# Optimization experiments

Hardware: AMD Instinct MI355X
Metric: run time of the kernel (lower is better)

Reference implementation:

```python
import jax, jax.numpy as jnp
import numpy as np

D_MODEL = 1024
NHEAD = 16
D_HEAD = D_MODEL // NHEAD


def setup_inputs() -> dict:
    key = jax.random.key(0)
    ks = jax.random.split(key, 11)
    B, S = 4, 1024
    s = 1.0 / np.sqrt(D_MODEL)
    inp = {
        'q_in': jax.random.normal(ks[0], (B, S, D_MODEL), jnp.float32),
        'k_in': jax.random.normal(ks[1], (B, S, D_MODEL), jnp.float32),
        'v_in': jax.random.normal(ks[2], (B, S, D_MODEL), jnp.float32),
        'Wq': jax.random.normal(ks[3], (D_MODEL, D_MODEL), jnp.float32) * s,
        'bq': jnp.zeros((D_MODEL,), jnp.float32),
        'Wk': jax.random.normal(ks[4], (D_MODEL, D_MODEL), jnp.float32) * s,
        'bk': jnp.zeros((D_MODEL,), jnp.float32),
        'Wv': jax.random.normal(ks[5], (D_MODEL, D_MODEL), jnp.float32) * s,
        'bv': jnp.zeros((D_MODEL,), jnp.float32),
        'Wo': jax.random.normal(ks[6], (D_MODEL, D_MODEL), jnp.float32) * s,
        'bo': jnp.zeros((D_MODEL,), jnp.float32),
    }
    return inp


def reference(q_in, k_in, v_in, Wq, bq, Wk, bk, Wv, bv, Wo, bo):
    B, Sq, _ = q_in.shape
    Sk = k_in.shape[1]
    # Linear projections (torch Linear: x @ W.T + b; here W stored as [in, out])
    Q = q_in @ Wq + bq
    K = k_in @ Wk + bk
    V = v_in @ Wv + bv
    # [B, H, S, Dh]
    Qh = Q.reshape(B, Sq, NHEAD, D_HEAD).transpose(0, 2, 1, 3)
    Kh = K.reshape(B, Sk, NHEAD, D_HEAD).transpose(0, 2, 1, 3)
    Vh = V.reshape(B, Sk, NHEAD, D_HEAD).transpose(0, 2, 1, 3)
    scores = jnp.einsum('bhqd,bhkd->bhqk', Qh, Kh) / jnp.sqrt(jnp.float32(D_HEAD))
    attn_weights = jax.nn.softmax(scores, axis=-1)
    attn = jnp.einsum('bhqk,bhkd->bhqd', attn_weights, Vh)
    attn = attn.transpose(0, 2, 1, 3).reshape(B, Sq, D_MODEL)
    out = attn @ Wo + bo
    return out
```

## Files before the change

### kernel.cpp

```cpp
#include <hip/hip_runtime.h>
#include <hip/hip_bf16.h>
#include <cstdint>
#include <cstddef>

typedef __bf16 bf16_t;
typedef __bf16 bf16x8 __attribute__((ext_vector_type(8)));
typedef __bf16 bf16x4 __attribute__((ext_vector_type(4)));
typedef float f32x4 __attribute__((ext_vector_type(4)));

#define DM 1024
#define NHEAD 16
#define DHEAD 64

#define QSCALE 0.18033688011112042f
#define PSHIFT 4.0f
#define RS 72

__device__ __forceinline__ void gload_lds16(const void* g, void* l) {
    __builtin_amdgcn_global_load_lds(
        (const __attribute__((address_space(1))) void*)g,
        (__attribute__((address_space(3))) void*)l,
        16, 0, 0);
}

__global__ void cast3_f32_to_bf16(
    const float* __restrict__ x0, const float* __restrict__ x1, const float* __restrict__ x2,
    bf16_t* __restrict__ y0, bf16_t* __restrict__ y1, bf16_t* __restrict__ y2, int n)
{
    const float* x = blockIdx.z == 0 ? x0 : blockIdx.z == 1 ? x1 : x2;
    bf16_t* y      = blockIdx.z == 0 ? y0 : blockIdx.z == 1 ? y1 : y2;
    int i = (blockIdx.x * blockDim.x + threadIdx.x) * 4;
    if (i < n) {
        float4 v = *(const float4*)&x[i];
        union { bf16_t b[4]; ushort4 u; } o;
        o.b[0] = (bf16_t)v.x; o.b[1] = (bf16_t)v.y; o.b[2] = (bf16_t)v.z; o.b[3] = (bf16_t)v.w;
        *(ushort4*)&y[i] = o.u;
    }
}

__global__ void transpose_cast_w4(
    const float* __restrict__ w0, const float* __restrict__ w1,
    const float* __restrict__ w2, const float* __restrict__ w3,
    bf16_t* __restrict__ t0, bf16_t* __restrict__ t1,
    bf16_t* __restrict__ t2, bf16_t* __restrict__ t3)
{
    const float* w = blockIdx.z == 0 ? w0 : blockIdx.z == 1 ? w1 : blockIdx.z == 2 ? w2 : w3;
    bf16_t* wt     = blockIdx.z == 0 ? t0 : blockIdx.z == 1 ? t1 : blockIdx.z == 2 ? t2 : t3;
    __shared__ float tile[32][33];
    int bx = blockIdx.x * 32;
    int by = blockIdx.y * 32;
    int tx = threadIdx.x, ty = threadIdx.y;
    for (int j = 0; j < 32; j += 8)
        tile[ty + j][tx] = w[(size_t)(by + ty + j) * DM + bx + tx];
    __syncthreads();
    for (int j = 0; j < 32; j += 8)
        wt[(size_t)(bx + ty + j) * DM + by + tx] = (bf16_t)tile[tx][ty + j];
}

template <int MODE>
__device__ __forceinline__ void gemm_body(
    const bf16_t* __restrict__ A, const bf16_t* __restrict__ Bt,
    const float* __restrict__ bias, float scale,
    float* __restrict__ Cf, bf16_t* __restrict__ Cb,
    int r0, int c0, bf16_t* AsP, bf16_t* BsP)
{
    const int K = 1024;
    int tid  = threadIdx.x;
    int wave = tid >> 6;
    int lane = tid & 63;
    int quad = lane >> 4;
    int ln   = lane & 15;
    int wr   = wave >> 1;
    int wc   = wave & 1;

    f32x4 acc[4][4];
    for (int rb = 0; rb < 4; rb++)
        for (int cb = 0; cb < 4; cb++)
            acc[rb][cb] = (f32x4){0.f, 0.f, 0.f, 0.f};

    int sr = tid >> 2;
    int sk = (tid & 3) * 8;

    const bf16_t* gA0 = &A[(size_t)(r0 + sr) * K + sk];
    const bf16_t* gA1 = gA0 + (size_t)64 * K;
    const bf16_t* gB0 = &Bt[(size_t)(c0 + sr) * K + sk];
    const bf16_t* gB1 = gB0 + (size_t)64 * K;
    char* lA = (char*)AsP + wave * 1024;
    char* lB = (char*)BsP + wave * 1024;

    for (int k0 = 0; k0 < K; k0 += 32) {
        __syncthreads();
        gload_lds16(gA0 + k0, lA);
        gload_lds16(gA1 + k0, lA + 4096);
        gload_lds16(gB0 + k0, lB);
        gload_lds16(gB1 + k0, lB + 4096);
        __syncthreads();

        bf16x8 af[4], bfv[4];
        for (int rb = 0; rb < 4; rb++)
            af[rb] = *(const bf16x8*)&AsP[(wr * 64 + rb * 16 + ln) * 32 + quad * 8];
        for (int cb = 0; cb < 4; cb++)
            bfv[cb] = *(const bf16x8*)&BsP[(wc * 64 + cb * 16 + ln) * 32 + quad * 8];
        for (int rb = 0; rb < 4; rb++)
            for (int cb = 0; cb < 4; cb++)
                acc[rb][cb] = __builtin_amdgcn_mfma_f32_16x16x32_bf16(af[rb], bfv[cb], acc[rb][cb], 0, 0, 0);
    }

    for (int rb = 0; rb < 4; rb++) {
        for (int cb = 0; cb < 4; cb++) {
            int C = c0 + wc * 64 + cb * 16 + ln;
            for (int r = 0; r < 4; r++) {
                int R = r0 + wr * 64 + rb * 16 + quad * 4 + r;
                float v = acc[rb][cb][r];
                if (MODE == 0) {
                    Cf[(size_t)R * DM + C] = v + bias[C];
                } else if (MODE == 1) {
                    int b = R >> 10, s = R & 1023;
                    int h = C >> 6,  d = C & 63;
                    Cb[(((size_t)b * NHEAD + h) * 1024 + s) * DHEAD + d] =
                        (bf16_t)((v + bias[C]) * scale);
                } else {
                    Cb[((size_t)(C >> 10) * 1024 + R) * 1024 + (C & 1023)] =
                        (bf16_t)(v + bias[R]);
                }
            }
        }
    }
}

__global__ __launch_bounds__(256) void gemm_qkv(
    const bf16_t* __restrict__ Xq, const bf16_t* __restrict__ Xk, const bf16_t* __restrict__ Xv,
    const bf16_t* __restrict__ Wtq, const bf16_t* __restrict__ Wtk, const bf16_t* __restrict__ Wtv,
    const float* __restrict__ bq, const float* __restrict__ bk, const float* __restrict__ bv,
    bf16_t* __restrict__ Qd, bf16_t* __restrict__ Kd, bf16_t* __restrict__ Vt)
{
    __shared__ __align__(16) bf16_t As[128 * 32];
    __shared__ __align__(16) bf16_t Bs[128 * 32];
    int z = blockIdx.z;
    if (z == 0) {
        gemm_body<1>(Xq, Wtq, bq, QSCALE, nullptr, Qd,
                     blockIdx.y * 128, blockIdx.x * 128, As, Bs);
    } else if (z == 1) {
        gemm_body<1>(Xk, Wtk, bk, 1.0f, nullptr, Kd,
                     blockIdx.y * 128, blockIdx.x * 128, As, Bs);
    } else {
        gemm_body<2>(Wtv, Xv, bv, 1.0f, nullptr, Vt,
                     blockIdx.x * 128, blockIdx.y * 128, As, Bs);
    }
}

__global__ __launch_bounds__(256) void gemm_out(
    const bf16_t* __restrict__ At, const bf16_t* __restrict__ Wto,
    const float* __restrict__ bo, float* __restrict__ out)
{
    __shared__ __align__(16) bf16_t As[128 * 32];
    __shared__ __align__(16) bf16_t Bs[128 * 32];
    gemm_body<0>(At, Wto, bo, 1.0f, out, nullptr,
                 blockIdx.y * 128, blockIdx.x * 128, As, Bs);
}

__global__ __launch_bounds__(256) void attn5(
    const bf16_t* __restrict__ Q,
    const bf16_t* __restrict__ K,
    const bf16_t* __restrict__ Vt,
    bf16_t* __restrict__ O)
{
    __shared__ __align__(16) bf16_t Ks[64 * RS];
    __shared__ __align__(16) bf16_t Vs[64 * RS];
    __shared__ __align__(16) bf16_t Ps[4][16 * RS];

    int tid  = threadIdx.x;
    int wave = tid >> 6;
    int lane = tid & 63;
    int quad = lane >> 4;
    int ln   = lane & 15;

    int bh = blockIdx.x;
    int q0w = blockIdx.y * 64 + wave * 16;

    const bf16_t* Qb = Q  + (size_t)bh * 65536;
    const bf16_t* Kb = K  + (size_t)bh * 65536;
    const bf16_t* Vb = Vt + (size_t)bh * 65536;

    int srow = tid >> 3;
    int scol = (tid & 7) * 8;
    const bf16_t* gK0 = Kb + (size_t)srow * 64 + scol;
    const bf16_t* gK1 = gK0 + 32 * 64;
    const bf16_t* gV0 = Vb + (size_t)srow * 1024 + scol;
    const bf16_t* gV1 = gV0 + 32 * 1024;

    bf16x8 aq0 = *(const bf16x8*)&Qb[(size_t)(q0w + ln) * 64 + quad * 8];
    bf16x8 aq1 = *(const bf16x8*)&Qb[(size_t)(q0w + ln) * 64 + 32 + quad * 8];

    uint4 rK0 = *(const uint4*)gK0;
    uint4 rK1 = *(const uint4*)gK1;
    uint4 rV0 = *(const uint4*)gV0;
    uint4 rV1 = *(const uint4*)gV1;

    float l_lane = 0.f;
    f32x4 o_acc[4];
    for (int cb = 0; cb < 4; cb++) o_acc[cb] = (f32x4){0.f, 0.f, 0.f, 0.f};

    bf16_t* Pw = Ps[wave];

    for (int kt = 0; kt < 16; kt++) {
        __syncthreads();
        *(uint4*)&Ks[srow * RS + scol]        = rK0;
        *(uint4*)&Ks[(32 + srow) * RS + scol] = rK1;
        *(uint4*)&Vs[srow * RS + scol]        = rV0;
        *(uint4*)&Vs[(32 + srow) * RS + scol] = rV1;
        __syncthreads();

        if (kt < 15) {
            gK0 += 4096; gK1 += 4096; gV0 += 64; gV1 += 64;
            rK0 = *(const uint4*)gK0;
            rK1 = *(const uint4*)gK1;
            rV0 = *(const uint4*)gV0;
            rV1 = *(const uint4*)gV1;
        }

        f32x4 sc[4];
        for (int kb = 0; kb < 4; kb++) {
            bf16x8 kf0 = *(const bf16x8*)&Ks[(kb * 16 + ln) * RS + quad * 8];
            bf16x8 kf1 = *(const bf16x8*)&Ks[(kb * 16 + ln) * RS + 32 + quad * 8];
            f32x4 a = (f32x4){0.f, 0.f, 0.f, 0.f};
            a = __builtin_amdgcn_mfma_f32_16x16x32_bf16(kf0, aq0, a, 0, 0, 0);
            a = __builtin_amdgcn_mfma_f32_16x16x32_bf16(kf1, aq1, a, 0, 0, 0);
            sc[kb] = a;
        }

        for (int kb = 0; kb < 4; kb++) {
            float p0 = __builtin_amdgcn_exp2f(sc[kb][0] - PSHIFT);
            float p1 = __builtin_amdgcn_exp2f(sc[kb][1] - PSHIFT);
            float p2 = __builtin_amdgcn_exp2f(sc[kb][2] - PSHIFT);
            float p3 = __builtin_amdgcn_exp2f(sc[kb][3] - PSHIFT);
            l_lane += (p0 + p1) + (p2 + p3);
            bf16x4 pk = (bf16x4){(bf16_t)p0, (bf16_t)p1, (bf16_t)p2, (bf16_t)p3};
            *(bf16x4*)&Pw[ln * RS + kb * 16 + quad * 4] = pk;
        }

        for (int kc = 0; kc < 2; kc++) {
            bf16x8 ap = *(const bf16x8*)&Pw[ln * RS + kc * 32 + quad * 8];
            for (int cb = 0; cb < 4; cb++) {
                bf16x8 vf = *(const bf16x8*)&Vs[(cb * 16 + ln) * RS + kc * 32 + quad * 8];
                o_acc[cb] = __builtin_amdgcn_mfma_f32_16x16x32_bf16(ap, vf, o_acc[cb], 0, 0, 0);
            }
        }
    }

    float l = l_lane;
    l += __shfl_xor(l, 16);
    l += __shfl_xor(l, 32);
    float invq[4];
    for (int r = 0; r < 4; r++)
        invq[r] = 1.f / __shfl(l, quad * 4 + r);

    int b = bh >> 4, h = bh & 15;
    for (int cb = 0; cb < 4; cb++) {
        for (int r = 0; r < 4; r++) {
            int q = q0w + quad * 4 + r;
            int d = cb * 16 + ln;
            O[((size_t)b * 1024 + q) * DM + h * 64 + d] = (bf16_t)(o_acc[cb][r] * invq[r]);
        }
    }
}

extern "C" void kernel_launch(void* const* d_in, const int* in_sizes, int n_in,
                              void* d_out, int out_size, void* d_ws, size_t ws_size,
                              hipStream_t stream) {
    const float* q_in = (const float*)d_in[0];
    const float* k_in = (const float*)d_in[1];
    const float* v_in = (const float*)d_in[2];
    const float* Wq   = (const float*)d_in[3];
    const float* bq   = (const float*)d_in[4];
    const float* Wk   = (const float*)d_in[5];
    const float* bk   = (const float*)d_in[6];
    const float* Wv   = (const float*)d_in[7];
    const float* bv   = (const float*)d_in[8];
    const float* Wo   = (const float*)d_in[9];
    const float* bo   = (const float*)d_in[10];

    char* ws = (char*)d_ws;
    const size_t MB = 1024ull * 1024ull;
    bf16_t* Xq  = (bf16_t*)(ws);
    bf16_t* Xk  = (bf16_t*)(ws + 8 * MB);
    bf16_t* Xv  = (bf16_t*)(ws + 16 * MB);
    bf16_t* Wtq = (bf16_t*)(ws + 24 * MB);
    bf16_t* Wtk = (bf16_t*)(ws + 26 * MB);
    bf16_t* Wtv = (bf16_t*)(ws + 28 * MB);
    bf16_t* Wto = (bf16_t*)(ws + 30 * MB);
    bf16_t* Qd  = (bf16_t*)(ws + 32 * MB);
    bf16_t* Kd  = (bf16_t*)(ws + 40 * MB);
    bf16_t* Vt  = (bf16_t*)(ws + 48 * MB);
    bf16_t* At  = Xq;

    const int nX = 4 * 1024 * DM;

    cast3_f32_to_bf16<<<dim3(nX / 4 / 256, 1, 3), 256, 0, stream>>>(
        q_in, k_in, v_in, Xq, Xk, Xv, nX);

    transpose_cast_w4<<<dim3(32, 32, 4), dim3(32, 8), 0, stream>>>(
        Wq, Wk, Wv, Wo, Wtq, Wtk, Wtv, Wto);

    gemm_qkv<<<dim3(8, 32, 3), 256, 0, stream>>>(Xq, Xk, Xv, Wtq, Wtk, Wtv, bq, bk, bv, Qd, Kd, Vt);

    attn5<<<dim3(64, 16), 256, 0, stream>>>(Qd, Kd, Vt, At);

    gemm_out<<<dim3(8, 32), 256, 0, stream>>>(At, Wto, bo, (float*)d_out);
}
```

Measured before the change: 231.8 us.

## Fuse f32-to-bf16 activation cast into QKV GEMM and retile output GEMM

Drops the separate cast kernel: the QKV GEMM now reads f32 activations directly, converts them to bf16 in registers and stores them to LDS, with register prefetch of the next K-slice. The block grid order is swapped so blocks sharing a weight column tile run adjacently. The output GEMM gets its own 64x128 tile kernel, which doubles the block count for better CU occupancy. The cost is a register-staged load path (no direct global-to-LDS) and twice the global read bytes for activations inside the GEMM.

```diff
diff --git a/kernel.cpp b/kernel.cpp
--- a/kernel.cpp
+++ b/kernel.cpp
@@ -23,19 +23,11 @@
         16, 0, 0);
 }
 
-__global__ void cast3_f32_to_bf16(
-    const float* __restrict__ x0, const float* __restrict__ x1, const float* __restrict__ x2,
-    bf16_t* __restrict__ y0, bf16_t* __restrict__ y1, bf16_t* __restrict__ y2, int n)
-{
-    const float* x = blockIdx.z == 0 ? x0 : blockIdx.z == 1 ? x1 : x2;
-    bf16_t* y      = blockIdx.z == 0 ? y0 : blockIdx.z == 1 ? y1 : y2;
-    int i = (blockIdx.x * blockDim.x + threadIdx.x) * 4;
-    if (i < n) {
-        float4 v = *(const float4*)&x[i];
-        union { bf16_t b[4]; ushort4 u; } o;
-        o.b[0] = (bf16_t)v.x; o.b[1] = (bf16_t)v.y; o.b[2] = (bf16_t)v.z; o.b[3] = (bf16_t)v.w;
-        *(ushort4*)&y[i] = o.u;
-    }
+__device__ __forceinline__ uint4 cvt8(float4 lo, float4 hi) {
+    union { bf16_t b[8]; uint4 u; } o;
+    o.b[0] = (bf16_t)lo.x; o.b[1] = (bf16_t)lo.y; o.b[2] = (bf16_t)lo.z; o.b[3] = (bf16_t)lo.w;
+    o.b[4] = (bf16_t)hi.x; o.b[5] = (bf16_t)hi.y; o.b[6] = (bf16_t)hi.z; o.b[7] = (bf16_t)hi.w;
+    return o.u;
 }
 
 __global__ void transpose_cast_w4(
@@ -57,9 +49,9 @@
         wt[(size_t)(bx + ty + j) * DM + by + tx] = (bf16_t)tile[tx][ty + j];
 }
 
-template <int MODE>
+template <int MODE, bool AF, bool BF>
 __device__ __forceinline__ void gemm_body(
-    const bf16_t* __restrict__ A, const bf16_t* __restrict__ Bt,
+    const void* __restrict__ Aop, const void* __restrict__ Bop,
     const float* __restrict__ bias, float scale,
     float* __restrict__ Cf, bf16_t* __restrict__ Cb,
     int r0, int c0, bf16_t* AsP, bf16_t* BsP)
@@ -81,20 +73,57 @@
     int sr = tid >> 2;
     int sk = (tid & 3) * 8;
 
-    const bf16_t* gA0 = &A[(size_t)(r0 + sr) * K + sk];
-    const bf16_t* gA1 = gA0 + (size_t)64 * K;
-    const bf16_t* gB0 = &Bt[(size_t)(c0 + sr) * K + sk];
-    const bf16_t* gB1 = gB0 + (size_t)64 * K;
+    const bf16_t* gA0h = AF ? nullptr : (const bf16_t*)Aop + (size_t)(r0 + sr) * K + sk;
+    const bf16_t* gA1h = AF ? nullptr : gA0h + (size_t)64 * K;
+    const bf16_t* gB0h = BF ? nullptr : (const bf16_t*)Bop + (size_t)(c0 + sr) * K + sk;
+    const bf16_t* gB1h = BF ? nullptr : gB0h + (size_t)64 * K;
+    const float* gA0f = AF ? (const float*)Aop + (size_t)(r0 + sr) * K + sk : nullptr;
+    const float* gA1f = AF ? gA0f + (size_t)64 * K : nullptr;
+    const float* gB0f = BF ? (const float*)Bop + (size_t)(c0 + sr) * K + sk : nullptr;
+    const float* gB1f = BF ? gB0f + (size_t)64 * K : nullptr;
+
     char* lA = (char*)AsP + wave * 1024;
     char* lB = (char*)BsP + wave * 1024;
 
+    float4 a0lo, a0hi, a1lo, a1hi;
+    float4 b0lo, b0hi, b1lo, b1hi;
+    if (AF) {
+        a0lo = *(const float4*)(gA0f);     a0hi = *(const float4*)(gA0f + 4);
+        a1lo = *(const float4*)(gA1f);     a1hi = *(const float4*)(gA1f + 4);
+    }
+    if (BF) {
+        b0lo = *(const float4*)(gB0f);     b0hi = *(const float4*)(gB0f + 4);
+        b1lo = *(const float4*)(gB1f);     b1hi = *(const float4*)(gB1f + 4);
+    }
+
     for (int k0 = 0; k0 < K; k0 += 32) {
         __syncthreads();
-        gload_lds16(gA0 + k0, lA);
-        gload_lds16(gA1 + k0, lA + 4096);
-        gload_lds16(gB0 + k0, lB);
-        gload_lds16(gB1 + k0, lB + 4096);
-        __syncthreads();
+        if (AF) {
+            *(uint4*)&AsP[sr * 32 + sk]        = cvt8(a0lo, a0hi);
+            *(uint4*)&AsP[(64 + sr) * 32 + sk] = cvt8(a1lo, a1hi);
+        } else {
+            gload_lds16(gA0h + k0, lA);
+            gload_lds16(gA1h + k0, lA + 4096);
+        }
+        if (BF) {
+            *(uint4*)&BsP[sr * 32 + sk]        = cvt8(b0lo, b0hi);
+            *(uint4*)&BsP[(64 + sr) * 32 + sk] = cvt8(b1lo, b1hi);
+        } else {
+            gload_lds16(gB0h + k0, lB);
+            gload_lds16(gB1h + k0, lB + 4096);
+        }
+        __syncthreads();
+
+        if (k0 + 32 < K) {
+            if (AF) {
+                a0lo = *(const float4*)(gA0f + k0 + 32);  a0hi = *(const float4*)(gA0f + k0 + 36);
+                a1lo = *(const float4*)(gA1f + k0 + 32);  a1hi = *(const float4*)(gA1f + k0 + 36);
+            }
+            if (BF) {
+                b0lo = *(const float4*)(gB0f + k0 + 32);  b0hi = *(const float4*)(gB0f + k0 + 36);
+                b1lo = *(const float4*)(gB1f + k0 + 32);  b1hi = *(const float4*)(gB1f + k0 + 36);
+            }
+        }
 
         bf16x8 af[4], bfv[4];
         for (int rb = 0; rb < 4; rb++)
@@ -129,7 +158,7 @@
 }
 
 __global__ __launch_bounds__(256) void gemm_qkv(
-    const bf16_t* __restrict__ Xq, const bf16_t* __restrict__ Xk, const bf16_t* __restrict__ Xv,
+    const float* __restrict__ Xq, const float* __restrict__ Xk, const float* __restrict__ Xv,
     const bf16_t* __restrict__ Wtq, const bf16_t* __restrict__ Wtk, const bf16_t* __restrict__ Wtv,
     const float* __restrict__ bq, const float* __restrict__ bk, const float* __restrict__ bv,
     bf16_t* __restrict__ Qd, bf16_t* __restrict__ Kd, bf16_t* __restrict__ Vt)
@@ -138,14 +167,14 @@
     __shared__ __align__(16) bf16_t Bs[128 * 32];
     int z = blockIdx.z;
     if (z == 0) {
-        gemm_body<1>(Xq, Wtq, bq, QSCALE, nullptr, Qd,
-                     blockIdx.y * 128, blockIdx.x * 128, As, Bs);
+        gemm_body<1, true, false>(Xq, Wtq, bq, QSCALE, nullptr, Qd,
+                                  blockIdx.x * 128, blockIdx.y * 128, As, Bs);
     } else if (z == 1) {
-        gemm_body<1>(Xk, Wtk, bk, 1.0f, nullptr, Kd,
-                     blockIdx.y * 128, blockIdx.x * 128, As, Bs);
+        gemm_body<1, true, false>(Xk, Wtk, bk, 1.0f, nullptr, Kd,
+                                  blockIdx.x * 128, blockIdx.y * 128, As, Bs);
     } else {
-        gemm_body<2>(Wtv, Xv, bv, 1.0f, nullptr, Vt,
-                     blockIdx.x * 128, blockIdx.y * 128, As, Bs);
+        gemm_body<2, false, true>(Wtv, Xv, bv, 1.0f, nullptr, Vt,
+                                  blockIdx.y * 128, blockIdx.x * 128, As, Bs);
     }
 }
 
@@ -153,10 +182,60 @@
     const bf16_t* __restrict__ At, const bf16_t* __restrict__ Wto,
     const float* __restrict__ bo, float* __restrict__ out)
 {
-    __shared__ __align__(16) bf16_t As[128 * 32];
+    const int K = 1024;
+    __shared__ __align__(16) bf16_t As[64 * 32];
     __shared__ __align__(16) bf16_t Bs[128 * 32];
-    gemm_body<0>(At, Wto, bo, 1.0f, out, nullptr,
-                 blockIdx.y * 128, blockIdx.x * 128, As, Bs);
+
+    int tid  = threadIdx.x;
+    int wave = tid >> 6;
+    int lane = tid & 63;
+    int quad = lane >> 4;
+    int ln   = lane & 15;
+
+    int r0 = blockIdx.x * 64;
+    int c0 = blockIdx.y * 128;
+
+    f32x4 acc[4][2];
+    for (int rb = 0; rb < 4; rb++)
+        for (int cb = 0; cb < 2; cb++)
+            acc[rb][cb] = (f32x4){0.f, 0.f, 0.f, 0.f};
+
+    int sr = tid >> 2;
+    int sk = (tid & 3) * 8;
+
+    const bf16_t* gA0 = At  + (size_t)(r0 + sr) * K + sk;
+    const bf16_t* gB0 = Wto + (size_t)(c0 + sr) * K + sk;
+    const bf16_t* gB1 = gB0 + (size_t)64 * K;
+    char* lA = (char*)As + wave * 1024;
+    char* lB = (char*)Bs + wave * 1024;
+
+    for (int k0 = 0; k0 < K; k0 += 32) {
+        __syncthreads();
+        gload_lds16(gA0 + k0, lA);
+        gload_lds16(gB0 + k0, lB);
+        gload_lds16(gB1 + k0, lB + 4096);
+        __syncthreads();
+
+        bf16x8 af[4], bfv[2];
+        for (int rb = 0; rb < 4; rb++)
+            af[rb] = *(const bf16x8*)&As[(rb * 16 + ln) * 32 + quad * 8];
+        for (int cb = 0; cb < 2; cb++)
+            bfv[cb] = *(const bf16x8*)&Bs[(wave * 32 + cb * 16 + ln) * 32 + quad * 8];
+        for (int rb = 0; rb < 4; rb++)
+            for (int cb = 0; cb < 2; cb++)
+                acc[rb][cb] = __builtin_amdgcn_mfma_f32_16x16x32_bf16(af[rb], bfv[cb], acc[rb][cb], 0, 0, 0);
+    }
+
+    for (int rb = 0; rb < 4; rb++) {
+        for (int cb = 0; cb < 2; cb++) {
+            int C = c0 + wave * 32 + cb * 16 + ln;
+            float bn = bo[C];
+            for (int r = 0; r < 4; r++) {
+                int R = r0 + rb * 16 + quad * 4 + r;
+                out[(size_t)R * DM + C] = acc[rb][cb][r] + bn;
+            }
+        }
+    }
 }
 
 __global__ __launch_bounds__(256) void attn5(
@@ -282,9 +361,7 @@
 
     char* ws = (char*)d_ws;
     const size_t MB = 1024ull * 1024ull;
-    bf16_t* Xq  = (bf16_t*)(ws);
-    bf16_t* Xk  = (bf16_t*)(ws + 8 * MB);
-    bf16_t* Xv  = (bf16_t*)(ws + 16 * MB);
+    bf16_t* At  = (bf16_t*)(ws);
     bf16_t* Wtq = (bf16_t*)(ws + 24 * MB);
     bf16_t* Wtk = (bf16_t*)(ws + 26 * MB);
     bf16_t* Wtv = (bf16_t*)(ws + 28 * MB);
@@ -292,19 +369,14 @@
     bf16_t* Qd  = (bf16_t*)(ws + 32 * MB);
     bf16_t* Kd  = (bf16_t*)(ws + 40 * MB);
     bf16_t* Vt  = (bf16_t*)(ws + 48 * MB);
-    bf16_t* At  = Xq;
-
-    const int nX = 4 * 1024 * DM;
-
-    cast3_f32_to_bf16<<<dim3(nX / 4 / 256, 1, 3), 256, 0, stream>>>(
-        q_in, k_in, v_in, Xq, Xk, Xv, nX);
 
     transpose_cast_w4<<<dim3(32, 32, 4), dim3(32, 8), 0, stream>>>(
         Wq, Wk, Wv, Wo, Wtq, Wtk, Wtv, Wto);
 
-    gemm_qkv<<<dim3(8, 32, 3), 256, 0, stream>>>(Xq, Xk, Xv, Wtq, Wtk, Wtv, bq, bk, bv, Qd, Kd, Vt);
+    gemm_qkv<<<dim3(32, 8, 3), 256, 0, stream>>>(q_in, k_in, v_in,
+                                                 Wtq, Wtk, Wtv, bq, bk, bv, Qd, Kd, Vt);
 
     attn5<<<dim3(64, 16), 256, 0, stream>>>(Qd, Kd, Vt, At);
 
-    gemm_out<<<dim3(8, 32), 256, 0, stream>>>(At, Wto, bo, (float*)d_out);
-}
+    gemm_out<<<dim3(64, 8), 256, 0, stream>>>(At, Wto, bo, (float*)d_out);
+}
```

Measured after the change: 231.5 us. About the same (-0.1%).
